# Optimization experiments

Hardware: AMD Instinct MI355X
Metric: run time of the kernel (lower is better)

The kernel has to match this reference:

```python
import jax, jax.numpy as jnp
import numpy as np

N = 10000      # nodes
E = 320000     # edges (avg degree 32)
DIN, H, DOUT = 4, 128, 16

# per-block MLP dims: (in, h1, h2, out); in = 2*feature_dim due to EdgeConv concat
_BLOCK_DIMS = [
    (2 * DIN, H, H, H),
    (2 * H,   H, H, H),
    (2 * H,   H, H, H),
    (2 * H,   H, H, DOUT),
]


def _mlp(h, Ws, bs):
    h = jax.nn.relu(h @ Ws[0] + bs[0])
    h = jax.nn.relu(h @ Ws[1] + bs[1])
    return h @ Ws[2] + bs[2]  # plain last layer


def _edgeconv(x, src, dst, Ws, bs):
    # PyG EdgeConv: message = nn(cat([x_i, x_j - x_i])), aggr='add' at target i
    xi = x[dst]              # [E, D] target features
    xj = x[src]              # [E, D] source features
    m = _mlp(jnp.concatenate([xi, xj - xi], axis=-1), Ws, bs)  # [E, Dout]
    return jax.ops.segment_sum(m, dst, num_segments=x.shape[0])


def setup_inputs() -> dict:
    key = jax.random.key(0)
    ks = iter(jax.random.split(key, 20))
    inp = {
        "x": jax.random.normal(next(ks), (N, DIN), jnp.float32),
        "pos": jax.random.normal(next(ks), (N, 3), jnp.float32),
        "edge_index": jax.random.randint(next(ks), (2, E), 0, N, dtype=jnp.int32),
        "batch": jnp.zeros((N,), jnp.int32),
    }
    for b, dims in enumerate(_BLOCK_DIMS):
        for l in range(3):
            inp[f"W{b}{l}"] = jax.random.normal(next(ks), (dims[l], dims[l + 1]), jnp.float32) / np.sqrt(dims[l]).astype(np.float32)
            inp[f"b{b}{l}"] = jnp.zeros((dims[l + 1],), jnp.float32)
    return inp


def reference(x, pos, edge_index, batch,
              W00, b00, W01, b01, W02, b02,
              W10, b10, W11, b11, W12, b12,
              W20, b20, W21, b21, W22, b22,
              W30, b30, W31, b31, W32, b32):
    src, dst = edge_index[0], edge_index[1]
    blocks = [
        ((W00, W01, W02), (b00, b01, b02)),
        ((W10, W11, W12), (b10, b11, b12)),
        ((W20, W21, W22), (b20, b21, b22)),
        ((W30, W31, W32), (b30, b31, b32)),
    ]
    for Ws, bs in blocks:
        x = _edgeconv(x, src, dst, Ws, bs)
    return x  # [N, DOUT]
```

## Files before the change

kernel.cpp:

```cpp
#include <hip/hip_runtime.h>
#include <hip/hip_bf16.h>

#define NN 10000
#define NE 320000
#define HD 128
#define TILE 128
#define NTILES (NE / TILE)

typedef __attribute__((ext_vector_type(8))) short s16x8;
typedef __attribute__((ext_vector_type(4))) short s16x4;
typedef __attribute__((ext_vector_type(4))) float f32x4;

__device__ __forceinline__ ushort f2bf(float f) {
    union { __hip_bfloat16 b; ushort u; } v;
    v.b = __float2bfloat16(f);
    return v.u;
}
__device__ __forceinline__ float bf2f(short s) {
    union { unsigned u; float f; } v;
    v.u = ((unsigned)(unsigned short)s) << 16;
    return v.f;
}

struct WPtrs { const float* w[8]; const float* w0[3]; };

__global__ __launch_bounds__(256)
void prep_kernel(const float* __restrict__ x, const float* __restrict__ W00,
                 const float* __restrict__ b00, ushort* __restrict__ A,
                 ushort* __restrict__ Bm, float* __restrict__ x0,
                 WPtrs p, ushort* __restrict__ wdst, int* __restrict__ cnt) {
    __shared__ float xs[16 * 128];
    const int blk = blockIdx.x;
    const int t = threadIdx.x;
    if (blk < 625) {
        const int n0 = blk * 16;
        for (int i = t; i < 16 * 4; i += 256) {
            int n = i / 4, d = i % 4;
            xs[n * 128 + d] = x[(size_t)(n0 + n) * 4 + d];
        }
        for (int i = t; i < 16 * 128; i += 256) x0[(size_t)n0 * 128 + i] = 0.f;
        __syncthreads();
        int c = t & 127;
        int h = t >> 7;
        float a[8], b[8];
        float bias = b00[c];
#pragma unroll
        for (int n = 0; n < 8; n++) { a[n] = bias; b[n] = 0.f; }
#pragma unroll
        for (int d = 0; d < 4; d++) {
            float wt = W00[d * HD + c];
            float wb = W00[(4 + d) * HD + c];
            float wd = wt - wb;
#pragma unroll
            for (int n = 0; n < 8; n++) {
                float xv = xs[(h * 8 + n) * 128 + d];
                a[n] += xv * wd;
                b[n] += xv * wb;
            }
        }
#pragma unroll
        for (int n = 0; n < 8; n++) {
            int gn = n0 + h * 8 + n;
            A[(size_t)gn * HD + c] = f2bf(a[n]);
            Bm[(size_t)gn * HD + c] = f2bf(b[n]);
        }
    } else if (blk < 1465) {
        int tid = (blk - 625) * 256 + t;
        if (tid < 7 * 16384) {
            int m = tid >> 14, idx = tid & 16383;
            int b = m >> 1, l = m & 1;
            int k = idx / 128, c = idx % 128;
            wdst[l * 65536 + b * 16384 + c * 128 + k] = f2bf(p.w[m][k * 128 + c]);
        } else if (tid < 7 * 16384 + 2048) {
            int idx = tid - 7 * 16384;
            int k = idx / 16, c = idx % 16;
            wdst[65536 + 3 * 16384 + c * 128 + k] = f2bf(p.w[7][k * 16 + c]);
        } else {
            int q = tid - 116736;
            int b = q >> 15, r = q & 32767;
            int cc = r >> 7, d = r & 127;
            const float* w0 = p.w0[b];
            float val = (cc < 128) ? (w0[d * 128 + cc] - w0[(128 + d) * 128 + cc])
                                   : w0[(128 + d) * 128 + (cc - 128)];
            wdst[131072 + b * 32768 + cc * 128 + d] = f2bf(val);
        }
    } else {
        int i = (blk - 1465) * 256 + t;
        if (i < NN) cnt[i] = 0;
    }
}

__global__ void hist_kernel(const int* __restrict__ dst, int* __restrict__ cnt) {
    int e = blockIdx.x * blockDim.x + threadIdx.x;
    if (e < NE) atomicAdd(&cnt[dst[e]], 1);
}

__global__ void scan_kernel(const int* __restrict__ cnt, int* __restrict__ rs, int* __restrict__ cur) {
    __shared__ int part[256];
    int t = threadIdx.x;
    const int CH = (NN + 255) / 256;
    int base = t * CH;
    int s = 0;
    for (int i = 0; i < CH; i++) {
        int idx = base + i;
        if (idx < NN) s += cnt[idx];
    }
    part[t] = s;
    __syncthreads();
    for (int off = 1; off < 256; off <<= 1) {
        int v = (t >= off) ? part[t - off] : 0;
        __syncthreads();
        part[t] += v;
        __syncthreads();
    }
    int run = part[t] - s;
    for (int i = 0; i < CH; i++) {
        int idx = base + i;
        if (idx < NN) {
            rs[idx] = run;
            cur[idx] = run;
            run += cnt[idx];
        }
    }
    if (t == 255) rs[NN] = run;
}

__global__ void scatter_kernel(const int* __restrict__ src, const int* __restrict__ dst,
                               int* __restrict__ cur, int* __restrict__ ssrc,
                               int* __restrict__ nof) {
    int e = blockIdx.x * blockDim.x + threadIdx.x;
    if (e < NE) {
        int d = dst[e];
        int p = atomicAdd(&cur[d], 1);
        ssrc[p] = src[e];
        nof[p] = d;
    }
}

__global__ __launch_bounds__(256)
void nodeAB_mfma_kernel(const float* __restrict__ xin, const ushort* __restrict__ WAB,
                        const float* __restrict__ b0, ushort* __restrict__ A,
                        ushort* __restrict__ Bm, float* __restrict__ zbuf, int ZD) {
    __shared__ __align__(16) ushort xs[32 * 136];
    const int t = threadIdx.x, lane = t & 63, w = t >> 6, lr = lane & 15, lg = lane >> 4;
    const int n0 = blockIdx.x * 32;

    for (int i = t; i < 1024; i += 256) {
        const int n = i >> 5, s4 = i & 31;
        const float4 xv = *(const float4*)(xin + (size_t)(n0 + n) * HD + s4 * 4);
        s16x4 hx;
        hx[0] = f2bf(xv.x); hx[1] = f2bf(xv.y); hx[2] = f2bf(xv.z); hx[3] = f2bf(xv.w);
        *(s16x4*)(xs + n * 136 + s4 * 4) = hx;
    }
    for (int i = t; i < 32 * ZD; i += 256) {
        const int n = i / ZD;
        if (n0 + n < NN) zbuf[(size_t)n0 * ZD + i] = 0.f;
    }
    __syncthreads();

    s16x8 wf[4][4];
#pragma unroll
    for (int nt = 0; nt < 4; nt++)
#pragma unroll
        for (int ks = 0; ks < 4; ks++)
            wf[nt][ks] = *(const s16x8*)(WAB + (size_t)(w * 64 + nt * 16 + lr) * HD + ks * 32 + lg * 8);

    f32x4 acc[2][4];
#pragma unroll
    for (int nt = 0; nt < 4; nt++) {
        const int cc = w * 64 + nt * 16 + lr;
        const float bb = (cc < 128) ? b0[cc] : 0.f;
        f32x4 v; v[0] = bb; v[1] = bb; v[2] = bb; v[3] = bb;
        acc[0][nt] = v;
        acc[1][nt] = v;
    }
#pragma unroll
    for (int ks = 0; ks < 4; ks++) {
#pragma unroll
        for (int g = 0; g < 2; g++) {
            const s16x8 xf = *(const s16x8*)(xs + (g * 16 + lr) * 136 + ks * 32 + lg * 8);
#pragma unroll
            for (int nt = 0; nt < 4; nt++)
                acc[g][nt] = __builtin_amdgcn_mfma_f32_16x16x32_bf16(xf, wf[nt][ks], acc[g][nt], 0, 0, 0);
        }
    }
#pragma unroll
    for (int g = 0; g < 2; g++)
#pragma unroll
        for (int nt = 0; nt < 4; nt++) {
            const int cc = w * 64 + nt * 16 + lr;
#pragma unroll
            for (int r = 0; r < 4; r++) {
                const int node = n0 + g * 16 + lg * 4 + r;
                if (node < NN) {
                    const ushort val = f2bf(acc[g][nt][r]);
                    if (cc < 128) A[(size_t)node * HD + cc] = val;
                    else Bm[(size_t)node * HD + (cc - 128)] = val;
                }
            }
        }
}

template<int DOUTB>
__global__ __launch_bounds__(256, 2)
void edge_mfma_kernel(const ushort* __restrict__ Af, const ushort* __restrict__ Bf,
                      const ushort* __restrict__ W1T, const float* __restrict__ b1,
                      const ushort* __restrict__ W2T, const float* __restrict__ b2,
                      const int* __restrict__ ssrc, const int* __restrict__ nof,
                      float* __restrict__ out) {
    __shared__ __align__(16) ushort HH1[TILE * 136];
    __shared__ __align__(16) ushort HH2[TILE * 136];
    __shared__ __align__(16) int s_node[2][TILE];

    const int t = threadIdx.x;
    const int lane = t & 63;
    const int w = t >> 6;
    const int lr = lane & 15;
    const int lg = lane >> 4;
    const int cg = t & 15;
    const int eb = t >> 4;

    s16x8 w1f[2][4];
#pragma unroll
    for (int m = 0; m < 2; m++)
#pragma unroll
        for (int ks = 0; ks < 4; ks++)
            w1f[m][ks] = *(const s16x8*)(W1T + (size_t)(w * 32 + m * 16 + lr) * HD + ks * 32 + lg * 8);

    constexpr int CT3 = (DOUTB == 128) ? 2 : 1;
    s16x8 w2f[CT3][4];
#pragma unroll
    for (int ct = 0; ct < CT3; ct++) {
        const int row = (DOUTB == 128) ? ((w * 2 + ct) * 16 + lr) : lr;
#pragma unroll
        for (int ks = 0; ks < 4; ks++)
            w2f[ct][ks] = *(const s16x8*)(W2T + (size_t)row * HD + ks * 32 + lg * 8);
    }

    float bias2[2][4];
#pragma unroll
    for (int m = 0; m < 2; m++)
#pragma unroll
        for (int r = 0; r < 4; r++)
            bias2[m][r] = b1[w * 32 + m * 16 + lg * 4 + r];
    float bias3[CT3];
#pragma unroll
    for (int ct = 0; ct < CT3; ct++)
        bias3[ct] = (DOUTB == 128) ? b2[(w * 2 + ct) * 16 + lr] : b2[lr];

    int tile = blockIdx.x;
    int ts = tile * TILE;
    if (t < TILE) s_node[0][t] = nof[ts + t];
    int nd[8], sr[8];
#pragma unroll
    for (int i = 0; i < 8; i++) {
        const int e = eb + 16 * i;
        nd[i] = nof[ts + e];
        sr[i] = ssrc[ts + e];
    }
    s16x8 bv[8];
#pragma unroll
    for (int i = 0; i < 8; i++)
        bv[i] = *(const s16x8*)(Bf + (size_t)sr[i] * HD + cg * 8);
    int buf = 0;
    __syncthreads();

    for (; tile < NTILES; tile += gridDim.x) {
        ts = tile * TILE;
        const int tn = (tile + (int)gridDim.x < NTILES) ? (tile + (int)gridDim.x) : tile;
        const int tsn = tn * TILE;

#pragma unroll
        for (int i = 0; i < 8; i++) {
            const int e = eb + 16 * i;
            const s16x8 av = *(const s16x8*)(Af + (size_t)nd[i] * HD + cg * 8);
            s16x8 hv;
#pragma unroll
            for (int j = 0; j < 8; j++)
                hv[j] = f2bf(fmaxf(bf2f(av[j]) + bf2f(bv[i][j]), 0.f));
            *(s16x8*)(HH1 + e * 136 + cg * 8) = hv;
        }
        __syncthreads();

#pragma unroll
        for (int i = 0; i < 8; i++) {
            const int e = eb + 16 * i;
            nd[i] = nof[tsn + e];
            sr[i] = ssrc[tsn + e];
        }
        if (t < TILE) s_node[buf ^ 1][t] = nof[tsn + t];

        f32x4 acc[2][8];
#pragma unroll
        for (int m = 0; m < 2; m++)
#pragma unroll
            for (int n = 0; n < 8; n++) {
                f32x4 v; v[0] = bias2[m][0]; v[1] = bias2[m][1]; v[2] = bias2[m][2]; v[3] = bias2[m][3];
                acc[m][n] = v;
            }
#pragma unroll
        for (int ks = 0; ks < 4; ks++) {
            const int k0 = ks * 32 + lg * 8;
            s16x8 bfr[8];
#pragma unroll
            for (int n = 0; n < 8; n++)
                bfr[n] = *(const s16x8*)(HH1 + (n * 16 + lr) * 136 + k0);
#pragma unroll
            for (int m = 0; m < 2; m++)
#pragma unroll
                for (int n = 0; n < 8; n++)
                    acc[m][n] = __builtin_amdgcn_mfma_f32_16x16x32_bf16(w1f[m][ks], bfr[n], acc[m][n], 0, 0, 0);
        }
#pragma unroll
        for (int m = 0; m < 2; m++)
#pragma unroll
            for (int n = 0; n < 8; n++) {
                const int e = n * 16 + lr;
                const int c0 = w * 32 + m * 16 + lg * 4;
                s16x4 hv;
                hv[0] = f2bf(fmaxf(acc[m][n][0], 0.f));
                hv[1] = f2bf(fmaxf(acc[m][n][1], 0.f));
                hv[2] = f2bf(fmaxf(acc[m][n][2], 0.f));
                hv[3] = f2bf(fmaxf(acc[m][n][3], 0.f));
                *(s16x4*)(HH2 + e * 136 + c0) = hv;
            }
#pragma unroll
        for (int i = 0; i < 8; i++)
            bv[i] = *(const s16x8*)(Bf + (size_t)sr[i] * HD + cg * 8);
        __syncthreads();

        if constexpr (DOUTB == 128) {
            f32x4 acc3[8][2];
#pragma unroll
            for (int n = 0; n < 8; n++)
#pragma unroll
                for (int ct = 0; ct < 2; ct++) {
                    const float bb = bias3[ct];
                    f32x4 v; v[0] = bb; v[1] = bb; v[2] = bb; v[3] = bb;
                    acc3[n][ct] = v;
                }
#pragma unroll
            for (int ks = 0; ks < 4; ks++) {
                const int k0 = ks * 32 + lg * 8;
                s16x8 h2f[8];
#pragma unroll
                for (int n = 0; n < 8; n++)
                    h2f[n] = *(const s16x8*)(HH2 + (n * 16 + lr) * 136 + k0);
#pragma unroll
                for (int n = 0; n < 8; n++)
#pragma unroll
                    for (int ct = 0; ct < 2; ct++)
                        acc3[n][ct] = __builtin_amdgcn_mfma_f32_16x16x32_bf16(h2f[n], w2f[ct][ks], acc3[n][ct], 0, 0, 0);
            }
#pragma unroll
            for (int n = 0; n < 8; n++)
#pragma unroll
                for (int ct = 0; ct < 2; ct++) {
                    const int e0 = n * 16 + lg * 4;
                    const int c = (w * 2 + ct) * 16 + lr;
                    s16x4 mv;
                    mv[0] = f2bf(acc3[n][ct][0]);
                    mv[1] = f2bf(acc3[n][ct][1]);
                    mv[2] = f2bf(acc3[n][ct][2]);
                    mv[3] = f2bf(acc3[n][ct][3]);
                    *(s16x4*)(HH1 + c * 136 + e0) = mv;
                }
        } else {
            f32x4 acc3[2];
#pragma unroll
            for (int e2 = 0; e2 < 2; e2++) {
                const float bb = bias3[0];
                f32x4 v; v[0] = bb; v[1] = bb; v[2] = bb; v[3] = bb;
                acc3[e2] = v;
            }
#pragma unroll
            for (int ks = 0; ks < 4; ks++) {
                const int k0 = ks * 32 + lg * 8;
#pragma unroll
                for (int e2 = 0; e2 < 2; e2++) {
                    const s16x8 h2f = *(const s16x8*)(HH2 + ((w * 2 + e2) * 16 + lr) * 136 + k0);
                    acc3[e2] = __builtin_amdgcn_mfma_f32_16x16x32_bf16(h2f, w2f[0][ks], acc3[e2], 0, 0, 0);
                }
            }
#pragma unroll
            for (int e2 = 0; e2 < 2; e2++) {
                const int e0 = (w * 2 + e2) * 16 + lg * 4;
                const int c = lr;
                s16x4 mv;
                mv[0] = f2bf(acc3[e2][0]);
                mv[1] = f2bf(acc3[e2][1]);
                mv[2] = f2bf(acc3[e2][2]);
                mv[3] = f2bf(acc3[e2][3]);
                *(s16x4*)(HH1 + c * 136 + e0) = mv;
            }
        }
        __syncthreads();

        const int* sn = s_node[buf];
        const int nd0 = sn[0];
        const int ndL = sn[TILE - 1];
        if constexpr (DOUTB == 128) {
            if (ndL - nd0 <= 15) {
                f32x4 agg[2];
                agg[0] = (f32x4)0.f; agg[1] = (f32x4)0.f;
#pragma unroll
                for (int ks = 0; ks < 4; ks++) {
                    const int4 na = *(const int4*)&sn[ks * 32 + lg * 8];
                    const int4 nb = *(const int4*)&sn[ks * 32 + lg * 8 + 4];
                    s16x8 sel;
                    sel[0] = (na.x - nd0 == lr) ? (short)0x3F80 : (short)0;
                    sel[1] = (na.y - nd0 == lr) ? (short)0x3F80 : (short)0;
                    sel[2] = (na.z - nd0 == lr) ? (short)0x3F80 : (short)0;
                    sel[3] = (na.w - nd0 == lr) ? (short)0x3F80 : (short)0;
                    sel[4] = (nb.x - nd0 == lr) ? (short)0x3F80 : (short)0;
                    sel[5] = (nb.y - nd0 == lr) ? (short)0x3F80 : (short)0;
                    sel[6] = (nb.z - nd0 == lr) ? (short)0x3F80 : (short)0;
                    sel[7] = (nb.w - nd0 == lr) ? (short)0x3F80 : (short)0;
#pragma unroll
                    for (int ci = 0; ci < 2; ci++) {
                        const s16x8 mf = *(const s16x8*)(HH1 + ((w * 2 + ci) * 16 + lr) * 136 + ks * 32 + lg * 8);
                        agg[ci] = __builtin_amdgcn_mfma_f32_16x16x32_bf16(sel, mf, agg[ci], 0, 0, 0);
                    }
                }
#pragma unroll
                for (int ci = 0; ci < 2; ci++) {
                    const int c = (w * 2 + ci) * 16 + lr;
#pragma unroll
                    for (int r = 0; r < 4; r++) {
                        const int ndn = nd0 + lg * 4 + r;
                        if (ndn <= ndL) {
                            float* dp = out + (size_t)ndn * 128 + c;
                            const float v = agg[ci][r];
                            if (ndn > nd0 && ndn < ndL) *dp = v;
                            else atomicAdd(dp, v);
                        }
                    }
                }
            } else {
                for (int idx = t; idx < TILE * 128; idx += 256) {
                    const int e = idx >> 7, c = idx & 127;
                    atomicAdd(out + (size_t)sn[e] * 128 + c, bf2f(HH1[c * 136 + e]));
                }
            }
        } else {
            const int nw0 = sn[w * 32];
            const int nwL = sn[w * 32 + 31];
            if (nwL - nw0 <= 15) {
                const int4 na = *(const int4*)&sn[w * 32 + lg * 8];
                const int4 nb = *(const int4*)&sn[w * 32 + lg * 8 + 4];
                s16x8 sel;
                sel[0] = (na.x - nw0 == lr) ? (short)0x3F80 : (short)0;
                sel[1] = (na.y - nw0 == lr) ? (short)0x3F80 : (short)0;
                sel[2] = (na.z - nw0 == lr) ? (short)0x3F80 : (short)0;
                sel[3] = (na.w - nw0 == lr) ? (short)0x3F80 : (short)0;
                sel[4] = (nb.x - nw0 == lr) ? (short)0x3F80 : (short)0;
                sel[5] = (nb.y - nw0 == lr) ? (short)0x3F80 : (short)0;
                sel[6] = (nb.z - nw0 == lr) ? (short)0x3F80 : (short)0;
                sel[7] = (nb.w - nw0 == lr) ? (short)0x3F80 : (short)0;
                const s16x8 mf = *(const s16x8*)(HH1 + lr * 136 + w * 32 + lg * 8);
                f32x4 agg = (f32x4)0.f;
                agg = __builtin_amdgcn_mfma_f32_16x16x32_bf16(sel, mf, agg, 0, 0, 0);
#pragma unroll
                for (int r = 0; r < 4; r++) {
                    const int ndn = nw0 + lg * 4 + r;
                    if (ndn <= nwL) {
                        float* dp = out + (size_t)ndn * 16 + lr;
                        const float v = agg[r];
                        if (ndn > nw0 && ndn < nwL) *dp = v;
                        else atomicAdd(dp, v);
                    }
                }
            } else {
                for (int idx = lane; idx < 32 * 16; idx += 64) {
                    const int e = w * 32 + (idx >> 4), c = idx & 15;
                    atomicAdd(out + (size_t)sn[e] * 16 + c, bf2f(HH1[c * 136 + e]));
                }
            }
        }
        buf ^= 1;
        __syncthreads();
    }
}

extern "C" void kernel_launch(void* const* d_in, const int* in_sizes, int n_in,
                              void* d_out, int out_size, void* d_ws, size_t ws_size,
                              hipStream_t stream) {
    const float* x = (const float*)d_in[0];
    const int* ei = (const int*)d_in[2];
    const int* src = ei;
    const int* dst = ei + NE;
    const float* W[4][3];
    const float* bs[4][3];
    for (int b = 0; b < 4; b++)
        for (int l = 0; l < 3; l++) {
            W[b][l]  = (const float*)d_in[4 + b * 6 + l * 2];
            bs[b][l] = (const float*)d_in[4 + b * 6 + l * 2 + 1];
        }

    float* x0   = (float*)d_ws;
    float* x1   = x0 + (size_t)NN * HD;
    ushort* A   = (ushort*)(x1 + (size_t)NN * HD);
    ushort* Bm  = A + (size_t)NN * HD;
    ushort* WT  = Bm + (size_t)NN * HD;
    int* cnt    = (int*)(WT + 229376);
    int* rs     = cnt + NN;
    int* cur    = rs + NN + 1;
    int* ssrc   = cur + NN;
    int* nof    = ssrc + NE;
    float* out  = (float*)d_out;

    WPtrs wp;
    for (int b = 0; b < 4; b++) { wp.w[2 * b] = W[b][1]; wp.w[2 * b + 1] = W[b][2]; }
    for (int b = 1; b < 4; b++) wp.w0[b - 1] = W[b][0];

    prep_kernel<<<1505, 256, 0, stream>>>(x, W[0][0], bs[0][0], A, Bm, x0, wp, WT, cnt);
    hist_kernel<<<(NE + 255) / 256, 256, 0, stream>>>(dst, cnt);
    scan_kernel<<<1, 256, 0, stream>>>(cnt, rs, cur);
    scatter_kernel<<<(NE + 255) / 256, 256, 0, stream>>>(src, dst, cur, ssrc, nof);

    const ushort* W1T[4];
    const ushort* W2T[4];
    const ushort* WAB[4];
    for (int b = 0; b < 4; b++) { W1T[b] = WT + b * 16384; W2T[b] = WT + 65536 + b * 16384; }
    for (int b = 1; b < 4; b++) WAB[b] = WT + 131072 + (b - 1) * 32768;

    const int EG = 500;

    edge_mfma_kernel<128><<<EG, 256, 0, stream>>>(A, Bm, W1T[0], bs[0][1], W2T[0], bs[0][2], ssrc, nof, x0);
    nodeAB_mfma_kernel<<<(NN + 31) / 32, 256, 0, stream>>>(x0, WAB[1], bs[1][0], A, Bm, x1, 128);
    edge_mfma_kernel<128><<<EG, 256, 0, stream>>>(A, Bm, W1T[1], bs[1][1], W2T[1], bs[1][2], ssrc, nof, x1);
    nodeAB_mfma_kernel<<<(NN + 31) / 32, 256, 0, stream>>>(x1, WAB[2], bs[2][0], A, Bm, x0, 128);
    edge_mfma_kernel<128><<<EG, 256, 0, stream>>>(A, Bm, W1T[2], bs[2][1], W2T[2], bs[2][2], ssrc, nof, x0);
    nodeAB_mfma_kernel<<<(NN + 31) / 32, 256, 0, stream>>>(x0, WAB[3], bs[3][0], A, Bm, out, 16);
    edge_mfma_kernel<16><<<EG, 256, 0, stream>>>(A, Bm, W1T[3], bs[3][1], W2T[3], bs[3][2], ssrc, nof, out);
}
```

Measured before the change: 259.3 us.

## Use 2x2 wave tiling for edge MLP MFMA layers instead of column split

```diff
diff --git a/kernel.cpp b/kernel.cpp
--- a/kernel.cpp
+++ b/kernel.cpp
@@ -217,36 +217,38 @@
     const int w = t >> 6;
     const int lr = lane & 15;
     const int lg = lane >> 4;
+    const int we = w >> 1;
+    const int wc = w & 1;
     const int cg = t & 15;
     const int eb = t >> 4;
 
-    s16x8 w1f[2][4];
-#pragma unroll
-    for (int m = 0; m < 2; m++)
+    s16x8 w1f[4][4];
+#pragma unroll
+    for (int mt = 0; mt < 4; mt++)
 #pragma unroll
         for (int ks = 0; ks < 4; ks++)
-            w1f[m][ks] = *(const s16x8*)(W1T + (size_t)(w * 32 + m * 16 + lr) * HD + ks * 32 + lg * 8);
-
-    constexpr int CT3 = (DOUTB == 128) ? 2 : 1;
+            w1f[mt][ks] = *(const s16x8*)(W1T + (size_t)(wc * 64 + mt * 16 + lr) * HD + ks * 32 + lg * 8);
+
+    constexpr int CT3 = (DOUTB == 128) ? 4 : 1;
     s16x8 w2f[CT3][4];
 #pragma unroll
     for (int ct = 0; ct < CT3; ct++) {
-        const int row = (DOUTB == 128) ? ((w * 2 + ct) * 16 + lr) : lr;
+        const int row = (DOUTB == 128) ? (wc * 64 + ct * 16 + lr) : lr;
 #pragma unroll
         for (int ks = 0; ks < 4; ks++)
             w2f[ct][ks] = *(const s16x8*)(W2T + (size_t)row * HD + ks * 32 + lg * 8);
     }
 
-    float bias2[2][4];
-#pragma unroll
-    for (int m = 0; m < 2; m++)
+    float bias2[4][4];
+#pragma unroll
+    for (int mt = 0; mt < 4; mt++)
 #pragma unroll
         for (int r = 0; r < 4; r++)
-            bias2[m][r] = b1[w * 32 + m * 16 + lg * 4 + r];
+            bias2[mt][r] = b1[wc * 64 + mt * 16 + lg * 4 + r];
     float bias3[CT3];
 #pragma unroll
     for (int ct = 0; ct < CT3; ct++)
-        bias3[ct] = (DOUTB == 128) ? b2[(w * 2 + ct) * 16 + lr] : b2[lr];
+        bias3[ct] = (DOUTB == 128) ? b2[wc * 64 + ct * 16 + lr] : b2[lr];
 
     int tile = blockIdx.x;
     int ts = tile * TILE;
@@ -290,38 +292,38 @@
         }
         if (t < TILE) s_node[buf ^ 1][t] = nof[tsn + t];
 
-        f32x4 acc[2][8];
-#pragma unroll
-        for (int m = 0; m < 2; m++)
-#pragma unroll
-            for (int n = 0; n < 8; n++) {
-                f32x4 v; v[0] = bias2[m][0]; v[1] = bias2[m][1]; v[2] = bias2[m][2]; v[3] = bias2[m][3];
-                acc[m][n] = v;
+        f32x4 acc[4][4];
+#pragma unroll
+        for (int mt = 0; mt < 4; mt++)
+#pragma unroll
+            for (int nt = 0; nt < 4; nt++) {
+                f32x4 v; v[0] = bias2[mt][0]; v[1] = bias2[mt][1]; v[2] = bias2[mt][2]; v[3] = bias2[mt][3];
+                acc[mt][nt] = v;
             }
 #pragma unroll
         for (int ks = 0; ks < 4; ks++) {
             const int k0 = ks * 32 + lg * 8;
-            s16x8 bfr[8];
-#pragma unroll
-            for (int n = 0; n < 8; n++)
-                bfr[n] = *(const s16x8*)(HH1 + (n * 16 + lr) * 136 + k0);
-#pragma unroll
-            for (int m = 0; m < 2; m++)
-#pragma unroll
-                for (int n = 0; n < 8; n++)
-                    acc[m][n] = __builtin_amdgcn_mfma_f32_16x16x32_bf16(w1f[m][ks], bfr[n], acc[m][n], 0, 0, 0);
-        }
-#pragma unroll
-        for (int m = 0; m < 2; m++)
-#pragma unroll
-            for (int n = 0; n < 8; n++) {
-                const int e = n * 16 + lr;
-                const int c0 = w * 32 + m * 16 + lg * 4;
+            s16x8 bfr[4];
+#pragma unroll
+            for (int nt = 0; nt < 4; nt++)
+                bfr[nt] = *(const s16x8*)(HH1 + (we * 64 + nt * 16 + lr) * 136 + k0);
+#pragma unroll
+            for (int mt = 0; mt < 4; mt++)
+#pragma unroll
+                for (int nt = 0; nt < 4; nt++)
+                    acc[mt][nt] = __builtin_amdgcn_mfma_f32_16x16x32_bf16(w1f[mt][ks], bfr[nt], acc[mt][nt], 0, 0, 0);
+        }
+#pragma unroll
+        for (int mt = 0; mt < 4; mt++)
+#pragma unroll
+            for (int nt = 0; nt < 4; nt++) {
+                const int e = we * 64 + nt * 16 + lr;
+                const int c0 = wc * 64 + mt * 16 + lg * 4;
                 s16x4 hv;
-                hv[0] = f2bf(fmaxf(acc[m][n][0], 0.f));
-                hv[1] = f2bf(fmaxf(acc[m][n][1], 0.f));
-                hv[2] = f2bf(fmaxf(acc[m][n][2], 0.f));
-                hv[3] = f2bf(fmaxf(acc[m][n][3], 0.f));
+                hv[0] = f2bf(fmaxf(acc[mt][nt][0], 0.f));
+                hv[1] = f2bf(fmaxf(acc[mt][nt][1], 0.f));
+                hv[2] = f2bf(fmaxf(acc[mt][nt][2], 0.f));
+                hv[3] = f2bf(fmaxf(acc[mt][nt][3], 0.f));
                 *(s16x4*)(HH2 + e * 136 + c0) = hv;
             }
 #pragma unroll
@@ -330,39 +332,39 @@
         __syncthreads();
 
         if constexpr (DOUTB == 128) {
-            f32x4 acc3[8][2];
-#pragma unroll
-            for (int n = 0; n < 8; n++)
-#pragma unroll
-                for (int ct = 0; ct < 2; ct++) {
+            f32x4 acc3[4][4];
+#pragma unroll
+            for (int nt = 0; nt < 4; nt++)
+#pragma unroll
+                for (int ct = 0; ct < 4; ct++) {
                     const float bb = bias3[ct];
                     f32x4 v; v[0] = bb; v[1] = bb; v[2] = bb; v[3] = bb;
-                    acc3[n][ct] = v;
+                    acc3[nt][ct] = v;
                 }
 #pragma unroll
             for (int ks = 0; ks < 4; ks++) {
                 const int k0 = ks * 32 + lg * 8;
-                s16x8 h2f[8];
-#pragma unroll
-                for (int n = 0; n < 8; n++)
-                    h2f[n] = *(const s16x8*)(HH2 + (n * 16 + lr) * 136 + k0);
-#pragma unroll
-                for (int n = 0; n < 8; n++)
-#pragma unroll
-                    for (int ct = 0; ct < 2; ct++)
-                        acc3[n][ct] = __builtin_amdgcn_mfma_f32_16x16x32_bf16(h2f[n], w2f[ct][ks], acc3[n][ct], 0, 0, 0);
-            }
-#pragma unroll
-            for (int n = 0; n < 8; n++)
-#pragma unroll
-                for (int ct = 0; ct < 2; ct++) {
-                    const int e0 = n * 16 + lg * 4;
-                    const int c = (w * 2 + ct) * 16 + lr;
+                s16x8 h2f[4];
+#pragma unroll
+                for (int nt = 0; nt < 4; nt++)
+                    h2f[nt] = *(const s16x8*)(HH2 + (we * 64 + nt * 16 + lr) * 136 + k0);
+#pragma unroll
+                for (int nt = 0; nt < 4; nt++)
+#pragma unroll
+                    for (int ct = 0; ct < 4; ct++)
+                        acc3[nt][ct] = __builtin_amdgcn_mfma_f32_16x16x32_bf16(h2f[nt], w2f[ct][ks], acc3[nt][ct], 0, 0, 0);
+            }
+#pragma unroll
+            for (int nt = 0; nt < 4; nt++)
+#pragma unroll
+                for (int ct = 0; ct < 4; ct++) {
+                    const int e0 = we * 64 + nt * 16 + lg * 4;
+                    const int c = wc * 64 + ct * 16 + lr;
                     s16x4 mv;
-                    mv[0] = f2bf(acc3[n][ct][0]);
-                    mv[1] = f2bf(acc3[n][ct][1]);
-                    mv[2] = f2bf(acc3[n][ct][2]);
-                    mv[3] = f2bf(acc3[n][ct][3]);
+                    mv[0] = f2bf(acc3[nt][ct][0]);
+                    mv[1] = f2bf(acc3[nt][ct][1]);
+                    mv[2] = f2bf(acc3[nt][ct][2]);
+                    mv[3] = f2bf(acc3[nt][ct][3]);
                     *(s16x4*)(HH1 + c * 136 + e0) = mv;
                 }
         } else {
```

Measured after the change: 424.6 us. 63.8% more time.
